# Kernel optimization log

Hardware: AMD Instinct MI355X
Metric: run time of the kernel (lower is better)

Reference implementation:

```python
import jax, jax.numpy as jnp
import numpy as np

N, E = 40000, 640000
IN_DIM, EDGE_DIM, HID, H1 = 5, 11, 128, 4
NEG_SLOPE = 0.2


def _add_self_loops(ei, ea, n):
    # PyG GATConv default: add_self_loops=True, fill_value='mean' for edge_attr
    loop = jnp.arange(n, dtype=ei.dtype)
    ei2 = jnp.concatenate([ei, jnp.stack([loop, loop])], axis=1)
    ea2 = jnp.concatenate([ea, jnp.broadcast_to(ea.mean(0), (n, ea.shape[1]))], axis=0)
    return ei2, ea2


def _gat(x, ei, ea, W, We, a_src, a_dst, a_edge, b, H, C):
    # Single GATConv layer (eval mode, dropout inactive)
    n = x.shape[0]
    xh = (x @ W).reshape(n, H, C)            # [N,H,C]
    eh = (ea @ We).reshape(-1, H, C)         # [E,H,C]
    src, dst = ei[0], ei[1]
    a_s = (xh * a_src).sum(-1)               # [N,H]
    a_d = (xh * a_dst).sum(-1)               # [N,H]
    alpha = jax.nn.leaky_relu(a_s[src] + a_d[dst] + (eh * a_edge).sum(-1), NEG_SLOPE)  # [E,H]
    amax = jax.ops.segment_max(alpha, dst, num_segments=n)
    ex = jnp.exp(alpha - amax[dst])
    den = jax.ops.segment_sum(ex, dst, num_segments=n)
    w = ex / (den[dst] + 1e-16)              # softmax over inbound edges per dst
    out = jax.ops.segment_sum(xh[src] * w[:, :, None], dst, num_segments=n)  # [N,H,C]
    return out.reshape(n, H * C) + b


def setup_inputs() -> dict:
    key = jax.random.key(0)
    ks = jax.random.split(key, 20)
    s = 0.1
    return {
        "x": jax.random.normal(ks[0], (N, IN_DIM), jnp.float32),
        "edge_index": jax.random.randint(ks[1], (2, E), 0, N),
        "edge_attr": jax.random.normal(ks[2], (E, EDGE_DIM), jnp.float32),
        "W1": jax.random.normal(ks[3], (IN_DIM, H1 * HID), jnp.float32) * s,
        "We1": jax.random.normal(ks[4], (EDGE_DIM, H1 * HID), jnp.float32) * s,
        "a_src1": jax.random.normal(ks[5], (H1, HID), jnp.float32) * s,
        "a_dst1": jax.random.normal(ks[6], (H1, HID), jnp.float32) * s,
        "a_edge1": jax.random.normal(ks[7], (H1, HID), jnp.float32) * s,
        "b1": jnp.zeros((H1 * HID,), jnp.float32),
        # layer 2 (512 -> 128, 1 head)
        "W2": jax.random.normal(ks[8], (H1 * HID, HID), jnp.float32) * s,
        "We2": jax.random.normal(ks[9], (EDGE_DIM, HID), jnp.float32) * s,
        "a_src2": jax.random.normal(ks[10], (1, HID), jnp.float32) * s,
        "a_dst2": jax.random.normal(ks[11], (1, HID), jnp.float32) * s,
        "a_edge2": jax.random.normal(ks[12], (1, HID), jnp.float32) * s,
        "b2": jnp.zeros((HID,), jnp.float32),
        # final linear 128 -> 1
        "Wfc": jax.random.normal(ks[13], (HID, 1), jnp.float32) * s,
        "bfc": jnp.zeros((1,), jnp.float32),
    }


def reference(x, edge_index, edge_attr,
              W1, We1, a_src1, a_dst1, a_edge1, b1,
              W2, We2, a_src2, a_dst2, a_edge2, b2,
              Wfc, bfc):
    ei, ea = _add_self_loops(edge_index, edge_attr, x.shape[0])
    h = jax.nn.relu(_gat(x, ei, ea, W1, We1, a_src1, a_dst1, a_edge1, b1, H1, HID))
    h = jax.nn.relu(_gat(h, ei, ea, W2, We2, a_src2, a_dst2, a_edge2, b2, 1, HID))
    return jax.nn.sigmoid(h @ Wfc + bfc)
```

## Files before the change

### kernel.cpp

```cpp
#include <hip/hip_runtime.h>

#define NN   40000
#define EE   640000
#define IND  5
#define ED   11
#define HIDD 128
#define F1   512
#define PSB  2500

typedef unsigned short u16;
typedef unsigned int   u32;
typedef __attribute__((ext_vector_type(8))) short bf16x8;
typedef __attribute__((ext_vector_type(4))) float f32x4;

__device__ __forceinline__ float bf2f(u16 u) { return __uint_as_float(((u32)u) << 16); }
__device__ __forceinline__ u16 f2bf(float f) {
    u32 u = __float_as_uint(f);
    return (u16)((u + 0x7FFFu + ((u >> 16) & 1u)) >> 16);
}

__device__ __forceinline__ float wsum(float v) {
#pragma unroll
    for (int o = 32; o; o >>= 1) v += __shfl_xor(v, o, 64);
    return v;
}
__device__ __forceinline__ float lrelu(float v) { return v > 0.f ? v : 0.2f * v; }


#define SBLK 256
#define SGRID ((NN + SBLK - 1) / SBLK)
#define PREPG (PSB + 33)

__global__ void __launch_bounds__(256) k_prep(const int* __restrict__ ei,
                                              int* __restrict__ counts,
                                              int* __restrict__ rank,
                                              float* __restrict__ consts,
                                              const float* __restrict__ ea,
                                              float* __restrict__ psum,
                                              const float* __restrict__ We1,
                                              const float* __restrict__ ae1,
                                              const float* __restrict__ We2,
                                              const float* __restrict__ ae2,
                                              const float* __restrict__ W2,
                                              u16* __restrict__ bsw,
                                              const float* __restrict__ W1,
                                              const float* __restrict__ as1,
                                              const float* __restrict__ ad1) {
    __shared__ float shf[4 * ED];
    int bid = blockIdx.x, t = threadIdx.x;
    if (bid < PSB) {
        int i = bid * 256 + t;
        rank[i] = atomicAdd(&counts[ei[EE + i]], 1);
        const float* row = ea + (size_t)i * ED;
        float r[ED];
#pragma unroll
        for (int k = 0; k < ED; ++k) r[k] = row[k];
#pragma unroll
        for (int k = 0; k < ED; ++k) r[k] = wsum(r[k]);
        int wv = t >> 6, lane = t & 63;
#pragma unroll
        for (int k = 0; k < ED; ++k)
            if (lane == k) shf[wv * ED + k] = r[k];
        __syncthreads();
        if (t < ED)
            psum[(size_t)bid * ED + t] =
                shf[t] + shf[ED + t] + shf[2 * ED + t] + shf[3 * ED + t];
        return;
    }
    if (bid == PSB) {
        if (t < 44) {
            int k = t >> 2, h = t & 3;
            float s = 0.f;
            for (int c = 0; c < HIDD; ++c)
                s += We1[k * F1 + h * HIDD + c] * ae1[h * HIDD + c];
            consts[16 + t] = s;
        }
        if (t >= 48 && t < 48 + ED) {
            int k = t - 48;
            float s = 0.f;
            for (int c = 0; c < HIDD; ++c)
                s += We2[k * HIDD + c] * ae2[c];
            consts[64 + k] = s;
        }
        if (t >= 64 && t < 84) {
            int idx = t - 64, j = idx >> 2, h = idx & 3;
            float s = 0.f;
            for (int c = 0; c < HIDD; ++c)
                s += W1[j * F1 + h * HIDD + c] * as1[h * HIDD + c];
            consts[100 + idx] = s;
        }
        if (t >= 84 && t < 104) {
            int idx = t - 84, j = idx >> 2, h = idx & 3;
            float s = 0.f;
            for (int c = 0; c < HIDD; ++c)
                s += W1[j * F1 + h * HIDD + c] * ad1[h * HIDD + c];
            consts[120 + idx] = s;
        }
        return;
    }
    int t2 = (bid - (PSB + 1)) * 256 + t;
    if (t2 >= 8192) return;
    int lane = t2 & 63, ks = (t2 >> 6) & 15, nt = t2 >> 10;
    int kbase = ks * 32 + (lane >> 4) * 8;
    int n = nt * 16 + (lane & 15);
    size_t dst = (size_t)t2 * 8;
#pragma unroll
    for (int j = 0; j < 8; ++j)
        bsw[dst + j] = f2bf(W2[(size_t)(kbase + j) * HIDD + n]);
}

__global__ void __launch_bounds__(SBLK) k_scan(const int* __restrict__ counts,
                                               int* __restrict__ row_off,
                                               const float* __restrict__ x,
                                               float* __restrict__ consts,
                                               float* __restrict__ gx,
                                               float* __restrict__ aD1,
                                               const float* __restrict__ psum) {
    __shared__ int shi[SBLK];
    __shared__ float shf[4 * ED];
    __shared__ float mean[ED];
    __shared__ int s_boff;
    int t = threadIdx.x, b = blockIdx.x;
    if (b < SGRID) {
        int acc = 0;
        for (int i = t; i < b * SBLK; i += SBLK) acc += counts[i];
        shi[t] = acc;
        __syncthreads();
        for (int o = 128; o; o >>= 1) {
            if (t < o) shi[t] += shi[t + o];
            __syncthreads();
        }
        if (t == 0) s_boff = shi[0];
        __syncthreads();
        int boff = s_boff;
        __syncthreads();
        int i = b * SBLK + t;
        int v = (i < NN) ? counts[i] : 0;
        shi[t] = v;
        __syncthreads();
        for (int o = 1; o < SBLK; o <<= 1) {
            int u = (t >= o) ? shi[t - o] : 0;
            __syncthreads();
            shi[t] += u;
            __syncthreads();
        }
        if (i < NN) row_off[i] = boff + shi[t] - v;
        if (b == 0 && t == 0) row_off[NN] = EE;
        return;
    }
    if (b == SGRID * 2) {
        float acc[ED];
#pragma unroll
        for (int k = 0; k < ED; ++k) acc[k] = 0.f;
        for (int w = t; w < PSB; w += SBLK) {
            const float* p = psum + (size_t)w * ED;
#pragma unroll
            for (int k = 0; k < ED; ++k) acc[k] += p[k];
        }
#pragma unroll
        for (int k = 0; k < ED; ++k) acc[k] = wsum(acc[k]);
        int wv = t >> 6, lane = t & 63;
#pragma unroll
        for (int k = 0; k < ED; ++k)
            if (lane == k) shf[wv * ED + k] = acc[k];
        __syncthreads();
        if (t < ED)
            mean[t] = (shf[t] + shf[ED + t] + shf[2 * ED + t] + shf[3 * ED + t])
                      * (1.0f / (float)EE);
        __syncthreads();
        if (t < 4) {
            float s = 0.f;
            for (int k = 0; k < ED; ++k) s += mean[k] * consts[16 + k * 4 + t];
            consts[80 + t] = s;
        }
        if (t == 8) {
            float s = 0.f;
            for (int k = 0; k < ED; ++k) s += mean[k] * consts[64 + k];
            consts[96] = s;
        }
        return;
    }
    int n = (b - SGRID) * SBLK + t;
    if (n >= NN) return;
    const float* xp = x + (size_t)n * IND;
    float xv0 = xp[0], xv1 = xp[1], xv2 = xp[2], xv3 = xp[3], xv4 = xp[4];
    float4 s4, d4;
    float* sp = (float*)&s4;
    float* dp = (float*)&d4;
#pragma unroll
    for (int h = 0; h < 4; ++h) {
        sp[h] = xv0 * consts[100 + 0 * 4 + h] + xv1 * consts[100 + 1 * 4 + h]
              + xv2 * consts[100 + 2 * 4 + h] + xv3 * consts[100 + 3 * 4 + h]
              + xv4 * consts[100 + 4 * 4 + h];
        dp[h] = xv0 * consts[120 + 0 * 4 + h] + xv1 * consts[120 + 1 * 4 + h]
              + xv2 * consts[120 + 2 * 4 + h] + xv3 * consts[120 + 3 * 4 + h]
              + xv4 * consts[120 + 4 * 4 + h];
    }
    float* gp = gx + (size_t)n * 12;
    *(float4*)gp = s4;
    float4 xq; xq.x = xv0; xq.y = xv1; xq.z = xv2; xq.w = xv3;
    *(float4*)(gp + 4) = xq;
    gp[8] = xv4;
    *(float4*)(aD1 + (size_t)n * 4) = d4;
}

__global__ void __launch_bounds__(256) k_build(const float* __restrict__ ea,
                                               const int* __restrict__ ei,
                                               const int* __restrict__ rank,
                                               const int* __restrict__ row_off,
                                               const float* __restrict__ consts,
                                               uint4* __restrict__ rec) {
    int t = threadIdx.x;
    int i = blockIdx.x * 256 + t;
    int s = ei[i];
    int d = ei[EE + i];
    int pos = row_off[d] + rank[i];
    const float* row = ea + (size_t)i * ED;
    float e0 = 0.f, e1 = 0.f, e2 = 0.f, e3 = 0.f, et = 0.f;
#pragma unroll
    for (int k = 0; k < ED; ++k) {
        float a = row[k];
        e0 += a * consts[16 + k * 4 + 0];
        e1 += a * consts[16 + k * 4 + 1];
        e2 += a * consts[16 + k * 4 + 2];
        e3 += a * consts[16 + k * 4 + 3];
        et += a * consts[64 + k];
    }
    uint4 q;
    q.x = (u32)f2bf(e0) | ((u32)f2bf(e1) << 16);
    q.y = (u32)f2bf(e2) | ((u32)f2bf(e3) << 16);
    q.z = (u32)s;
    q.w = __float_as_uint(et);
    rec[pos] = q;
}

__global__ void __launch_bounds__(256) k_agg1g(const int* __restrict__ row_off,
                                               const uint4* __restrict__ rec,
                                               const float* __restrict__ gx,
                                               const float* __restrict__ aD1,
                                               const float* __restrict__ W1,
                                               const float* __restrict__ b1,
                                               const float* __restrict__ consts,
                                               const u16* __restrict__ bsw,
                                               const float* __restrict__ as2,
                                               const float* __restrict__ ad2,
                                               u16* __restrict__ xh2,
                                               float* __restrict__ aS2,
                                               float* __restrict__ aD2) {
    __shared__ u16 hA[16 * 512];
    __shared__ float sh_ps[4][16], sh_pd[4][16];
    int wv = threadIdx.x >> 6, lane = threadIdx.x & 63;
    int g = lane >> 4, sl = lane & 15;
    int row = wv * 4 + g;
    int n0 = blockIdx.x * 16;
    int n = n0 + row;
    int s0 = row_off[n], s1 = row_off[n + 1];
    float4 adv = *(const float4*)(aD1 + (size_t)n * 4);
    float z0 = 0.f, z1 = 0.f, z2 = 0.f, z3 = 0.f;
    float xa[4][5];
#pragma unroll
    for (int h = 0; h < 4; ++h)
#pragma unroll
        for (int j = 0; j < 5; ++j) xa[h][j] = 0.f;

    int i = s0 + sl;
    uint4 q;
    if (i < s1) q = rec[i];
    while (i < s1) {
        int in2 = i + 16;
        uint4 qn;
        if (in2 < s1) qn = rec[in2];
        int s = (int)q.z;
        const float* gp = gx + (size_t)s * 12;
        float4 as4 = *(const float4*)gp;
        float4 xq  = *(const float4*)(gp + 4);
        float x4v  = gp[8];
        float e0 = bf2f((u16)(q.x & 0xFFFF)), e1 = bf2f((u16)(q.x >> 16));
        float e2 = bf2f((u16)(q.y & 0xFFFF)), e3 = bf2f((u16)(q.y >> 16));
        float ex;
        ex = __expf(lrelu(e0 + as4.x + adv.x)); z0 += ex;
        xa[0][0] += ex * xq.x; xa[0][1] += ex * xq.y; xa[0][2] += ex * xq.z;
        xa[0][3] += ex * xq.w; xa[0][4] += ex * x4v;
        ex = __expf(lrelu(e1 + as4.y + adv.y)); z1 += ex;
        xa[1][0] += ex * xq.x; xa[1][1] += ex * xq.y; xa[1][2] += ex * xq.z;
        xa[1][3] += ex * xq.w; xa[1][4] += ex * x4v;
        ex = __expf(lrelu(e2 + as4.z + adv.z)); z2 += ex;
        xa[2][0] += ex * xq.x; xa[2][1] += ex * xq.y; xa[2][2] += ex * xq.z;
        xa[2][3] += ex * xq.w; xa[2][4] += ex * x4v;
        ex = __expf(lrelu(e3 + as4.w + adv.w)); z3 += ex;
        xa[3][0] += ex * xq.x; xa[3][1] += ex * xq.y; xa[3][2] += ex * xq.z;
        xa[3][3] += ex * xq.w; xa[3][4] += ex * x4v;
        i = in2; q = qn;
    }
    if (sl == 0) {
        const float* gp = gx + (size_t)n * 12;
        float4 as4 = *(const float4*)gp;
        float4 xq  = *(const float4*)(gp + 4);
        float x4v  = gp[8];
        float ex;
        ex = __expf(lrelu(consts[80] + as4.x + adv.x)); z0 += ex;
        xa[0][0] += ex * xq.x; xa[0][1] += ex * xq.y; xa[0][2] += ex * xq.z;
        xa[0][3] += ex * xq.w; xa[0][4] += ex * x4v;
        ex = __expf(lrelu(consts[81] + as4.y + adv.y)); z1 += ex;
        xa[1][0] += ex * xq.x; xa[1][1] += ex * xq.y; xa[1][2] += ex * xq.z;
        xa[1][3] += ex * xq.w; xa[1][4] += ex * x4v;
        ex = __expf(lrelu(consts[82] + as4.z + adv.z)); z2 += ex;
        xa[2][0] += ex * xq.x; xa[2][1] += ex * xq.y; xa[2][2] += ex * xq.z;
        xa[2][3] += ex * xq.w; xa[2][4] += ex * x4v;
        ex = __expf(lrelu(consts[83] + as4.w + adv.w)); z3 += ex;
        xa[3][0] += ex * xq.x; xa[3][1] += ex * xq.y; xa[3][2] += ex * xq.z;
        xa[3][3] += ex * xq.w; xa[3][4] += ex * x4v;
    }
#pragma unroll
    for (int o = 1; o <= 8; o <<= 1) {
        z0 += __shfl_xor(z0, o, 64); z1 += __shfl_xor(z1, o, 64);
        z2 += __shfl_xor(z2, o, 64); z3 += __shfl_xor(z3, o, 64);
#pragma unroll
        for (int h = 0; h < 4; ++h)
#pragma unroll
            for (int j = 0; j < 5; ++j) xa[h][j] += __shfl_xor(xa[h][j], o, 64);
    }
    float zz[4] = {z0, z1, z2, z3};
#pragma unroll
    for (int cb = 0; cb < 4; ++cb) {
        float ih = 1.f / (zz[cb] + 1e-16f);
        int c0 = cb * 128 + sl * 8;
        u32 wp[4];
#pragma unroll
        for (int jj = 0; jj < 4; ++jj) {
            int c = c0 + jj * 2;
            float v0 = (xa[cb][0] * W1[0 * F1 + c] + xa[cb][1] * W1[1 * F1 + c]
                      + xa[cb][2] * W1[2 * F1 + c] + xa[cb][3] * W1[3 * F1 + c]
                      + xa[cb][4] * W1[4 * F1 + c]) * ih;
            float v1 = (xa[cb][0] * W1[0 * F1 + c + 1] + xa[cb][1] * W1[1 * F1 + c + 1]
                      + xa[cb][2] * W1[2 * F1 + c + 1] + xa[cb][3] * W1[3 * F1 + c + 1]
                      + xa[cb][4] * W1[4 * F1 + c + 1]) * ih;
            v0 = fmaxf(v0 + b1[c], 0.f);
            v1 = fmaxf(v1 + b1[c + 1], 0.f);
            wp[jj] = (u32)f2bf(v0) | ((u32)f2bf(v1) << 16);
        }
        uint4 st; st.x = wp[0]; st.y = wp[1]; st.z = wp[2]; st.w = wp[3];
        int cbyte = (cb * 256 + sl * 16) ^ ((row & 7) << 4);
        *(uint4*)((char*)hA + row * 1024 + cbyte) = st;
    }
    __syncthreads();

    int mrow = lane & 15, quad = lane >> 4;
    const u16* bbase = bsw + lane * 8;
    int nt0 = wv * 2;
    f32x4 acc0 = (f32x4){0.f, 0.f, 0.f, 0.f};
    f32x4 acc1 = (f32x4){0.f, 0.f, 0.f, 0.f};
    const char* arow = (const char*)hA + mrow * 1024;
    int axor = (mrow & 7) << 4;
    bf16x8 af0 = *(const bf16x8*)(arow + ((quad * 16 + 0) ^ axor));
    bf16x8 af1;
    bf16x8 b00 = *(const bf16x8*)(bbase + (size_t)nt0 * 8192);
    bf16x8 b01 = *(const bf16x8*)(bbase + (size_t)(nt0 + 1) * 8192);
    bf16x8 n00, n01;
#pragma unroll
    for (int ks = 0; ks < 16; ++ks) {
        if (ks < 15) {
            af1 = *(const bf16x8*)(arow + ((quad * 16 + (ks + 1) * 64) ^ axor));
            n00 = *(const bf16x8*)(bbase + (size_t)nt0 * 8192 + (ks + 1) * 512);
            n01 = *(const bf16x8*)(bbase + (size_t)(nt0 + 1) * 8192 + (ks + 1) * 512);
        }
        acc0 = __builtin_amdgcn_mfma_f32_16x16x32_bf16(af0, b00, acc0, 0, 0, 0);
        acc1 = __builtin_amdgcn_mfma_f32_16x16x32_bf16(af0, b01, acc1, 0, 0, 0);
        af0 = af1; b00 = n00; b01 = n01;
    }
    float ps[4] = {0.f, 0.f, 0.f, 0.f}, pd[4] = {0.f, 0.f, 0.f, 0.f};
    {
        int col = nt0 * 16 + mrow;
        float sa = as2[col], da = ad2[col];
#pragma unroll
        for (int r = 0; r < 4; ++r) {
            float v = acc0[r];
            xh2[(size_t)(n0 + quad * 4 + r) * HIDD + col] = f2bf(v);
            ps[r] += v * sa; pd[r] += v * da;
        }
    }
    {
        int col = (nt0 + 1) * 16 + mrow;
        float sa = as2[col], da = ad2[col];
#pragma unroll
        for (int r = 0; r < 4; ++r) {
            float v = acc1[r];
            xh2[(size_t)(n0 + quad * 4 + r) * HIDD + col] = f2bf(v);
            ps[r] += v * sa; pd[r] += v * da;
        }
    }
#pragma unroll
    for (int r = 0; r < 4; ++r) {
#pragma unroll
        for (int o = 1; o <= 8; o <<= 1) {
            ps[r] += __shfl_xor(ps[r], o, 64);
            pd[r] += __shfl_xor(pd[r], o, 64);
        }
        if (mrow == 0) {
            sh_ps[wv][quad * 4 + r] = ps[r];
            sh_pd[wv][quad * 4 + r] = pd[r];
        }
    }
    __syncthreads();
    int t = threadIdx.x;
    if (t < 16) {
        float s = sh_ps[0][t] + sh_ps[1][t] + sh_ps[2][t] + sh_ps[3][t];
        aS2[n0 + t] = s;
    } else if (t < 32) {
        int r = t - 16;
        float s = sh_pd[0][r] + sh_pd[1][r] + sh_pd[2][r] + sh_pd[3][r];
        aD2[n0 + r] = s;
    }
}

__global__ void __launch_bounds__(256) k_agg2(const int* __restrict__ row_off,
                                              const uint4* __restrict__ rec,
                                              const float* __restrict__ aS2,
                                              const float* __restrict__ aD2,
                                              const u16* __restrict__ xh2,
                                              const float* __restrict__ bias2,
                                              const float* __restrict__ Wfc,
                                              const float* __restrict__ bfc,
                                              const float* __restrict__ consts,
                                              float* __restrict__ out) {
    int n = blockIdx.x * 4 + (threadIdx.x >> 6);
    int t = threadIdx.x & 63;
    int s0 = row_off[n], s1 = row_off[n + 1];
    float adn = aD2[n];
    int g = t >> 4, l = t & 15;
    int c0 = l * 8;
    float z = 0.f;
    float acc[8];
#pragma unroll
    for (int j = 0; j < 8; ++j) acc[j] = 0.f;
    int i = s0 + g;
    uint4 qe;
    if (i < s1) qe = rec[i];
    while (i < s1) {
        int in2 = i + 4;
        uint4 qn;
        if (in2 < s1) qn = rec[in2];
        int s = (int)qe.z;
        float et2 = __uint_as_float(qe.w);
        float ex = __expf(lrelu(aS2[s] + adn + et2));
        z += ex;
        uint4 q = *(const uint4*)(xh2 + (size_t)s * HIDD + c0);
        acc[0] += ex * bf2f((u16)(q.x & 0xFFFF)); acc[1] += ex * bf2f((u16)(q.x >> 16));
        acc[2] += ex * bf2f((u16)(q.y & 0xFFFF)); acc[3] += ex * bf2f((u16)(q.y >> 16));
        acc[4] += ex * bf2f((u16)(q.z & 0xFFFF)); acc[5] += ex * bf2f((u16)(q.z >> 16));
        acc[6] += ex * bf2f((u16)(q.w & 0xFFFF)); acc[7] += ex * bf2f((u16)(q.w >> 16));
        i = in2; qe = qn;
    }
    if (g == 0) {
        float ex = __expf(lrelu(aS2[n] + adn + consts[96]));
        z += ex;
        uint4 q = *(const uint4*)(xh2 + (size_t)n * HIDD + c0);
        acc[0] += ex * bf2f((u16)(q.x & 0xFFFF)); acc[1] += ex * bf2f((u16)(q.x >> 16));
        acc[2] += ex * bf2f((u16)(q.y & 0xFFFF)); acc[3] += ex * bf2f((u16)(q.y >> 16));
        acc[4] += ex * bf2f((u16)(q.z & 0xFFFF)); acc[5] += ex * bf2f((u16)(q.z >> 16));
        acc[6] += ex * bf2f((u16)(q.w & 0xFFFF)); acc[7] += ex * bf2f((u16)(q.w >> 16));
    }
#pragma unroll
    for (int o = 16; o <= 32; o <<= 1) {
        z += __shfl_xor(z, o, 64);
#pragma unroll
        for (int j = 0; j < 8; ++j) acc[j] += __shfl_xor(acc[j], o, 64);
    }
    float inv = 1.f / (z + 1e-16f);
    float p = 0.f;
#pragma unroll
    for (int j = 0; j < 8; ++j) {
        float o = fmaxf(acc[j] * inv + bias2[c0 + j], 0.f);
        p += o * Wfc[c0 + j];
    }
#pragma unroll
    for (int o = 1; o <= 8; o <<= 1) p += __shfl_xor(p, o, 64);
    if (t == 0) {
        float logit = p + bfc[0];
        out[n] = 1.f / (1.f + __expf(-logit));
    }
}

extern "C" void kernel_launch(void* const* d_in, const int* in_sizes, int n_in,
                              void* d_out, int out_size, void* d_ws, size_t ws_size,
                              hipStream_t stream) {
    (void)in_sizes; (void)n_in; (void)out_size; (void)ws_size;
    const float* x   = (const float*)d_in[0];
    const int*   ei  = (const int*)d_in[1];
    const float* ea  = (const float*)d_in[2];
    const float* W1  = (const float*)d_in[3];
    const float* We1 = (const float*)d_in[4];
    const float* as1 = (const float*)d_in[5];
    const float* ad1 = (const float*)d_in[6];
    const float* ae1 = (const float*)d_in[7];
    const float* b1  = (const float*)d_in[8];
    const float* W2  = (const float*)d_in[9];
    const float* We2 = (const float*)d_in[10];
    const float* as2 = (const float*)d_in[11];
    const float* ad2 = (const float*)d_in[12];
    const float* ae2 = (const float*)d_in[13];
    const float* b2v = (const float*)d_in[14];
    const float* Wfc = (const float*)d_in[15];
    const float* bfc = (const float*)d_in[16];
    float* out = (float*)d_out;

    char* ws = (char*)d_ws;
    size_t off = 0;
    auto take = [&](size_t nb) {
        size_t r = off;
        off += (nb + 255) & ~(size_t)255;
        return r;
    };
    float* consts = (float*)(ws + take(1024));
    int*   counts = (int*)(ws + take((size_t)NN * 4));
    size_t zbytes = off;
    int* row_off  = (int*)(ws + take((size_t)(NN + 1) * 4));
    int* rank     = (int*)(ws + take((size_t)EE * 4));
    float* psum   = (float*)(ws + take((size_t)PSB * ED * 4));
    uint4* rec    = (uint4*)(ws + take((size_t)EE * 16));
    float* gx     = (float*)(ws + take((size_t)NN * 48));
    float* aD1    = (float*)(ws + take((size_t)NN * 16));
    float* aS2    = (float*)(ws + take((size_t)NN * 4));
    float* aD2    = (float*)(ws + take((size_t)NN * 4));
    u16* xh2      = (u16*)(ws + take((size_t)NN * HIDD * 2));
    u16* w2b      = (u16*)(ws + take((size_t)65536 * 2));

    hipMemsetAsync(ws, 0, zbytes, stream);
    k_prep<<<PREPG, 256, 0, stream>>>(ei, counts, rank, consts, ea, psum,
                                      We1, ae1, We2, ae2, W2, w2b, W1, as1, ad1);
    k_scan<<<SGRID * 2 + 1, SBLK, 0, stream>>>(counts, row_off, x, consts,
                                               gx, aD1, psum);
    k_build<<<PSB, 256, 0, stream>>>(ea, ei, rank, row_off, consts, rec);
    k_agg1g<<<PSB, 256, 0, stream>>>(row_off, rec, gx, aD1, W1, b1, consts,
                                     w2b, as2, ad2, xh2, aS2, aD2);
    k_agg2<<<NN / 4, 256, 0, stream>>>(row_off, rec, aS2, aD2, xh2, b2v, Wfc, bfc,
                                       consts, out);
}
```

Before: 237.3 us.

## Fuse edge projection into prep kernel and move node precompute out of scan

Edge-attribute projections are computed in k_prep, where each edge row is already loaded for the mean. Each block rebuilds the projection constants in shared memory, and the packed record goes to a temporary buffer that k_build only scatters. Node-level gx/aD1 computation moves from k_scan into extra k_prep blocks. This avoids rereading edge_attr in k_build, at the cost of a temporary buffer round trip and redundant per-block constant dot products.

Result: slower. 252.3 us (+6.3%).

```diff
diff --git a/kernel.cpp b/kernel.cpp
--- a/kernel.cpp
+++ b/kernel.cpp
@@ -29,7 +29,7 @@
 
 #define SBLK 256
 #define SGRID ((NN + SBLK - 1) / SBLK)
-#define PREPG (PSB + 33)
+#define PREPG (PSB + 33 + SGRID)
 
 __global__ void __launch_bounds__(256) k_prep(const int* __restrict__ ei,
                                               int* __restrict__ counts,
@@ -37,6 +37,7 @@
                                               float* __restrict__ consts,
                                               const float* __restrict__ ea,
                                               float* __restrict__ psum,
+                                              uint4* __restrict__ tmp,
                                               const float* __restrict__ We1,
                                               const float* __restrict__ ae1,
                                               const float* __restrict__ We2,
@@ -45,16 +46,53 @@
                                               u16* __restrict__ bsw,
                                               const float* __restrict__ W1,
                                               const float* __restrict__ as1,
-                                              const float* __restrict__ ad1) {
-    __shared__ float shf[4 * ED];
+                                              const float* __restrict__ ad1,
+                                              const float* __restrict__ x,
+                                              float* __restrict__ gx,
+                                              float* __restrict__ aD1) {
     int bid = blockIdx.x, t = threadIdx.x;
     if (bid < PSB) {
+        __shared__ float shB[64];
+        __shared__ float shf[4 * ED];
         int i = bid * 256 + t;
-        rank[i] = atomicAdd(&counts[ei[EE + i]], 1);
+        int d = ei[EE + i];
+        int rk = atomicAdd(&counts[d], 1);
+        if (t < 44) {
+            int k = t >> 2, h = t & 3;
+            float s = 0.f;
+            for (int c = 0; c < HIDD; ++c)
+                s += We1[k * F1 + h * HIDD + c] * ae1[h * HIDD + c];
+            shB[t] = s;
+        }
+        if (t >= 48 && t < 48 + ED) {
+            int k = t - 48;
+            float s = 0.f;
+            for (int c = 0; c < HIDD; ++c)
+                s += We2[k * HIDD + c] * ae2[c];
+            shB[t] = s;
+        }
+        __syncthreads();
+        rank[i] = rk;
         const float* row = ea + (size_t)i * ED;
         float r[ED];
 #pragma unroll
         for (int k = 0; k < ED; ++k) r[k] = row[k];
+        float e0 = 0.f, e1 = 0.f, e2 = 0.f, e3 = 0.f, et = 0.f;
+#pragma unroll
+        for (int k = 0; k < ED; ++k) {
+            float a = r[k];
+            e0 += a * shB[k * 4 + 0];
+            e1 += a * shB[k * 4 + 1];
+            e2 += a * shB[k * 4 + 2];
+            e3 += a * shB[k * 4 + 3];
+            et += a * shB[48 + k];
+        }
+        uint4 q;
+        q.x = (u32)f2bf(e0) | ((u32)f2bf(e1) << 16);
+        q.y = (u32)f2bf(e2) | ((u32)f2bf(e3) << 16);
+        q.z = (u32)ei[i];
+        q.w = __float_as_uint(et);
+        tmp[i] = q;
 #pragma unroll
         for (int k = 0; k < ED; ++k) r[k] = wsum(r[k]);
         int wv = t >> 6, lane = t & 63;
@@ -82,39 +120,63 @@
                 s += We2[k * HIDD + c] * ae2[c];
             consts[64 + k] = s;
         }
-        if (t >= 64 && t < 84) {
-            int idx = t - 64, j = idx >> 2, h = idx & 3;
+        return;
+    }
+    if (bid < PSB + 33) {
+        int t2 = (bid - (PSB + 1)) * 256 + t;
+        if (t2 >= 8192) return;
+        int lane = t2 & 63, ks = (t2 >> 6) & 15, nt = t2 >> 10;
+        int kbase = ks * 32 + (lane >> 4) * 8;
+        int n = nt * 16 + (lane & 15);
+        size_t dst = (size_t)t2 * 8;
+#pragma unroll
+        for (int j = 0; j < 8; ++j)
+            bsw[dst + j] = f2bf(W2[(size_t)(kbase + j) * HIDD + n]);
+        return;
+    }
+    {
+        __shared__ float sA[20], sD[20];
+        if (t < 20) {
+            int j = t >> 2, h = t & 3;
             float s = 0.f;
             for (int c = 0; c < HIDD; ++c)
                 s += W1[j * F1 + h * HIDD + c] * as1[h * HIDD + c];
-            consts[100 + idx] = s;
-        }
-        if (t >= 84 && t < 104) {
-            int idx = t - 84, j = idx >> 2, h = idx & 3;
+            sA[t] = s;
+        }
+        if (t >= 32 && t < 52) {
+            int u = t - 32, j = u >> 2, h = u & 3;
             float s = 0.f;
             for (int c = 0; c < HIDD; ++c)
                 s += W1[j * F1 + h * HIDD + c] * ad1[h * HIDD + c];
-            consts[120 + idx] = s;
-        }
-        return;
-    }
-    int t2 = (bid - (PSB + 1)) * 256 + t;
-    if (t2 >= 8192) return;
-    int lane = t2 & 63, ks = (t2 >> 6) & 15, nt = t2 >> 10;
-    int kbase = ks * 32 + (lane >> 4) * 8;
-    int n = nt * 16 + (lane & 15);
-    size_t dst = (size_t)t2 * 8;
-#pragma unroll
-    for (int j = 0; j < 8; ++j)
-        bsw[dst + j] = f2bf(W2[(size_t)(kbase + j) * HIDD + n]);
+            sD[u] = s;
+        }
+        __syncthreads();
+        int n = (bid - (PSB + 33)) * 256 + t;
+        if (n >= NN) return;
+        const float* xp = x + (size_t)n * IND;
+        float xv0 = xp[0], xv1 = xp[1], xv2 = xp[2], xv3 = xp[3], xv4 = xp[4];
+        float4 s4, d4;
+        float* sp = (float*)&s4;
+        float* dp = (float*)&d4;
+#pragma unroll
+        for (int h = 0; h < 4; ++h) {
+            sp[h] = xv0 * sA[0 * 4 + h] + xv1 * sA[1 * 4 + h] + xv2 * sA[2 * 4 + h]
+                  + xv3 * sA[3 * 4 + h] + xv4 * sA[4 * 4 + h];
+            dp[h] = xv0 * sD[0 * 4 + h] + xv1 * sD[1 * 4 + h] + xv2 * sD[2 * 4 + h]
+                  + xv3 * sD[3 * 4 + h] + xv4 * sD[4 * 4 + h];
+        }
+        float* gp = gx + (size_t)n * 12;
+        *(float4*)gp = s4;
+        float4 xq; xq.x = xv0; xq.y = xv1; xq.z = xv2; xq.w = xv3;
+        *(float4*)(gp + 4) = xq;
+        gp[8] = xv4;
+        *(float4*)(aD1 + (size_t)n * 4) = d4;
+    }
 }
 
 __global__ void __launch_bounds__(SBLK) k_scan(const int* __restrict__ counts,
                                                int* __restrict__ row_off,
-                                               const float* __restrict__ x,
                                                float* __restrict__ consts,
-                                               float* __restrict__ gx,
-                                               float* __restrict__ aD1,
                                                const float* __restrict__ psum) {
     __shared__ int shi[SBLK];
     __shared__ float shf[4 * ED];
@@ -148,90 +210,46 @@
         if (b == 0 && t == 0) row_off[NN] = EE;
         return;
     }
-    if (b == SGRID * 2) {
-        float acc[ED];
-#pragma unroll
-        for (int k = 0; k < ED; ++k) acc[k] = 0.f;
-        for (int w = t; w < PSB; w += SBLK) {
-            const float* p = psum + (size_t)w * ED;
-#pragma unroll
-            for (int k = 0; k < ED; ++k) acc[k] += p[k];
-        }
-#pragma unroll
-        for (int k = 0; k < ED; ++k) acc[k] = wsum(acc[k]);
-        int wv = t >> 6, lane = t & 63;
-#pragma unroll
-        for (int k = 0; k < ED; ++k)
-            if (lane == k) shf[wv * ED + k] = acc[k];
-        __syncthreads();
-        if (t < ED)
-            mean[t] = (shf[t] + shf[ED + t] + shf[2 * ED + t] + shf[3 * ED + t])
-                      * (1.0f / (float)EE);
-        __syncthreads();
-        if (t < 4) {
-            float s = 0.f;
-            for (int k = 0; k < ED; ++k) s += mean[k] * consts[16 + k * 4 + t];
-            consts[80 + t] = s;
-        }
-        if (t == 8) {
-            float s = 0.f;
-            for (int k = 0; k < ED; ++k) s += mean[k] * consts[64 + k];
-            consts[96] = s;
-        }
-        return;
-    }
-    int n = (b - SGRID) * SBLK + t;
-    if (n >= NN) return;
-    const float* xp = x + (size_t)n * IND;
-    float xv0 = xp[0], xv1 = xp[1], xv2 = xp[2], xv3 = xp[3], xv4 = xp[4];
-    float4 s4, d4;
-    float* sp = (float*)&s4;
-    float* dp = (float*)&d4;
-#pragma unroll
-    for (int h = 0; h < 4; ++h) {
-        sp[h] = xv0 * consts[100 + 0 * 4 + h] + xv1 * consts[100 + 1 * 4 + h]
-              + xv2 * consts[100 + 2 * 4 + h] + xv3 * consts[100 + 3 * 4 + h]
-              + xv4 * consts[100 + 4 * 4 + h];
-        dp[h] = xv0 * consts[120 + 0 * 4 + h] + xv1 * consts[120 + 1 * 4 + h]
-              + xv2 * consts[120 + 2 * 4 + h] + xv3 * consts[120 + 3 * 4 + h]
-              + xv4 * consts[120 + 4 * 4 + h];
-    }
-    float* gp = gx + (size_t)n * 12;
-    *(float4*)gp = s4;
-    float4 xq; xq.x = xv0; xq.y = xv1; xq.z = xv2; xq.w = xv3;
-    *(float4*)(gp + 4) = xq;
-    gp[8] = xv4;
-    *(float4*)(aD1 + (size_t)n * 4) = d4;
-}
-
-__global__ void __launch_bounds__(256) k_build(const float* __restrict__ ea,
+    float acc[ED];
+#pragma unroll
+    for (int k = 0; k < ED; ++k) acc[k] = 0.f;
+    for (int w = t; w < PSB; w += SBLK) {
+        const float* p = psum + (size_t)w * ED;
+#pragma unroll
+        for (int k = 0; k < ED; ++k) acc[k] += p[k];
+    }
+#pragma unroll
+    for (int k = 0; k < ED; ++k) acc[k] = wsum(acc[k]);
+    int wv = t >> 6, lane = t & 63;
+#pragma unroll
+    for (int k = 0; k < ED; ++k)
+        if (lane == k) shf[wv * ED + k] = acc[k];
+    __syncthreads();
+    if (t < ED)
+        mean[t] = (shf[t] + shf[ED + t] + shf[2 * ED + t] + shf[3 * ED + t])
+                  * (1.0f / (float)EE);
+    __syncthreads();
+    if (t < 4) {
+        float s = 0.f;
+        for (int k = 0; k < ED; ++k) s += mean[k] * consts[16 + k * 4 + t];
+        consts[80 + t] = s;
+    }
+    if (t == 8) {
+        float s = 0.f;
+        for (int k = 0; k < ED; ++k) s += mean[k] * consts[64 + k];
+        consts[96] = s;
+    }
+}
+
+__global__ void __launch_bounds__(256) k_build(const uint4* __restrict__ tmp,
                                                const int* __restrict__ ei,
                                                const int* __restrict__ rank,
                                                const int* __restrict__ row_off,
-                                               const float* __restrict__ consts,
                                                uint4* __restrict__ rec) {
-    int t = threadIdx.x;
-    int i = blockIdx.x * 256 + t;
-    int s = ei[i];
+    int i = blockIdx.x * 256 + threadIdx.x;
+    uint4 q = tmp[i];
     int d = ei[EE + i];
-    int pos = row_off[d] + rank[i];
-    const float* row = ea + (size_t)i * ED;
-    float e0 = 0.f, e1 = 0.f, e2 = 0.f, e3 = 0.f, et = 0.f;
-#pragma unroll
-    for (int k = 0; k < ED; ++k) {
-        float a = row[k];
-        e0 += a * consts[16 + k * 4 + 0];
-        e1 += a * consts[16 + k * 4 + 1];
-        e2 += a * consts[16 + k * 4 + 2];
-        e3 += a * consts[16 + k * 4 + 3];
-        et += a * consts[64 + k];
-    }
-    uint4 q;
-    q.x = (u32)f2bf(e0) | ((u32)f2bf(e1) << 16);
-    q.y = (u32)f2bf(e2) | ((u32)f2bf(e3) << 16);
-    q.z = (u32)s;
-    q.w = __float_as_uint(et);
-    rec[pos] = q;
+    rec[row_off[d] + rank[i]] = q;
 }
 
 __global__ void __launch_bounds__(256) k_agg1g(const int* __restrict__ row_off,
@@ -517,6 +535,7 @@
     int* row_off  = (int*)(ws + take((size_t)(NN + 1) * 4));
     int* rank     = (int*)(ws + take((size_t)EE * 4));
     float* psum   = (float*)(ws + take((size_t)PSB * ED * 4));
+    uint4* tmp    = (uint4*)(ws + take((size_t)EE * 16));
     uint4* rec    = (uint4*)(ws + take((size_t)EE * 16));
     float* gx     = (float*)(ws + take((size_t)NN * 48));
     float* aD1    = (float*)(ws + take((size_t)NN * 16));
@@ -526,11 +545,11 @@
     u16* w2b      = (u16*)(ws + take((size_t)65536 * 2));
 
     hipMemsetAsync(ws, 0, zbytes, stream);
-    k_prep<<<PREPG, 256, 0, stream>>>(ei, counts, rank, consts, ea, psum,
-                                      We1, ae1, We2, ae2, W2, w2b, W1, as1, ad1);
-    k_scan<<<SGRID * 2 + 1, SBLK, 0, stream>>>(counts, row_off, x, consts,
-                                               gx, aD1, psum);
-    k_build<<<PSB, 256, 0, stream>>>(ea, ei, rank, row_off, consts, rec);
+    k_prep<<<PREPG, 256, 0, stream>>>(ei, counts, rank, consts, ea, psum, tmp,
+                                      We1, ae1, We2, ae2, W2, w2b, W1, as1, ad1,
+                                      x, gx, aD1);
+    k_scan<<<SGRID + 1, SBLK, 0, stream>>>(counts, row_off, consts, psum);
+    k_build<<<PSB, 256, 0, stream>>>(tmp, ei, rank, row_off, rec);
     k_agg1g<<<PSB, 256, 0, stream>>>(row_off, rec, gx, aD1, W1, b1, consts,
                                      w2b, as2, ad2, xh2, aS2, aD2);
     k_agg2<<<NN / 4, 256, 0, stream>>>(row_off, rec, aS2, aD2, xh2, b2v, Wfc, bfc,
```
